# Optimization experiments

Measured on AMD Instinct MI355X. Metric: run time of the kernel, lower is better.

## Reference

```python
import jax, jax.numpy as jnp
import numpy as np

STRIDE = 1

def setup_inputs() -> dict:
    key = jax.random.key(0)
    k1, k2 = jax.random.split(key)
    x = jax.random.normal(k1, (16, 32, 32768), dtype=jnp.float32)
    # original uses torch.rand -> uniform [0,1)
    kernel = jax.random.uniform(k2, (1, 32, 32, 3), dtype=jnp.float32)
    return {"x": x, "kernel": kernel}

def reference(x, kernel):
    # Faithful intent of the module: strided valid 1D convolution.
    # x: (B, C_in, L); kernel: (1, C_out, C_in, K)
    w = kernel[0]  # (C_out, C_in, K)
    out = jax.lax.conv_general_dilated(
        x, w,
        window_strides=(STRIDE,),
        padding='VALID',
        dimension_numbers=('NCH', 'OIH', 'NCH'),
    )  # (B, C_out, (L-K)//STRIDE + 1)
    return out
```

## Files before the change

kernel.cpp:

```cpp
#include <hip/hip_runtime.h>

#define L_IN   32768
#define L_OUT  32766
#define C_IN   32
#define C_OUT  32
#define KW     3
#define TILE_L 128
#define TPB    4
#define NGRP   64
#define XROWS  130
#define PITCHW 32
#define LDSW   (XROWS * PITCHW)
#define WPLANE 3072

typedef __attribute__((ext_vector_type(8))) short bf16x8;
typedef __attribute__((ext_vector_type(4))) float f32x4;
typedef __attribute__((ext_vector_type(4))) unsigned int u32x4;

__device__ __forceinline__ unsigned pack_split(float v) {
    unsigned u = __float_as_uint(v);
    unsigned r = u + 0x7fffu + ((u >> 16) & 1u);
    float lo = v - __uint_as_float(r & 0xffff0000u);
    return (__float_as_uint(lo) & 0xffff0000u) | (r >> 16);
}

__device__ __forceinline__ unsigned prm(unsigned a, unsigned b, unsigned sel) {
    return __builtin_amdgcn_perm(a, b, sel);
}

__device__ __forceinline__ int lds_word(int l, int ci) {
    return l * PITCHW + ((((ci >> 2) ^ (l & 7)) << 2) | (ci & 3));
}

__global__ void prep_w(const float* __restrict__ w, unsigned short* __restrict__ wtf) {
    const int i = blockIdx.x * 256 + threadIdx.x;
    if (i >= 6 * 64 * 8) return;
    const int f    = i >> 9;
    const int rr   = i & 511;
    const int lane = rr >> 3;
    const int j    = rr & 7;
    const int kw   = f >> 1;
    const int cot  = f & 1;
    const int co   = cot * 16 + (lane & 15);
    const int ci   = (lane >> 4) * 8 + j;
    const float v  = w[(co * C_IN + ci) * KW + kw];
    unsigned u = __float_as_uint(v);
    unsigned r = u + 0x7fffu + ((u >> 16) & 1u);
    unsigned short hi = (unsigned short)(r >> 16);
    float lof = v - __uint_as_float(r & 0xffff0000u);
    unsigned lu = __float_as_uint(lof);
    unsigned lr = lu + 0x7fffu + ((lu >> 16) & 1u);
    unsigned short lo = (unsigned short)(lr >> 16);
    wtf[(f * 64 + lane) * 8 + j]          = hi;
    wtf[WPLANE + (f * 64 + lane) * 8 + j] = lo;
}

__global__ __launch_bounds__(256, 4) void conv1d_mfma(
    const float* __restrict__ x, const unsigned short* __restrict__ wtf,
    float* __restrict__ out)
{
    __shared__ __attribute__((aligned(16))) unsigned       xs[LDSW];
    __shared__ __attribute__((aligned(16))) unsigned short wl[2 * WPLANE];

    const int tid  = threadIdx.x;
    const int lane = tid & 63;
    const int wv   = tid >> 6;
    const int blk  = ((blockIdx.x & 7) << 7) | (blockIdx.x >> 3);
    const int bb   = blk >> 6;
    const int grp  = blk & (NGRP - 1);
    const int lg0  = grp * (TILE_L * TPB);

    const float* xb = x + (size_t)bb * C_IN * L_IN;

    {
        const u32x4* wsv = (const u32x4*)wtf;
        u32x4*       wdv = (u32x4*)wl;
#pragma unroll
        for (int i = 0; i < 3; ++i)
            wdv[tid * 3 + i] = wsv[tid * 3 + i];
    }

    const int c   = tid & 31;
    const int rr0 = tid >> 5;
    const int n   = lane & 15;
    const int kg  = lane >> 4;
    const int lb  = wv * 32;

    float sv[2][4][4];
    float hv[2];

    auto LOADT = [&](int l0, int s) {
#pragma unroll
        for (int r = 0; r < 4; ++r) {
            const float* src = xb + (size_t)(rr0 + r * 8) * L_IN + l0;
#pragma unroll
            for (int q = 0; q < 4; ++q)
                sv[s][r][q] = src[c + q * 32];
        }
        hv[s] = 0.f;
        if (tid < 64) {
            const int gl = l0 + TILE_L + (tid & 1);
            if (gl < L_IN) hv[s] = xb[(size_t)(tid >> 1) * L_IN + gl];
        }
        asm volatile("" ::: "memory");
    };
    auto WRITET = [&](int s) {
#pragma unroll
        for (int r = 0; r < 4; ++r)
#pragma unroll
            for (int q = 0; q < 4; ++q)
                xs[lds_word(c + q * 32, rr0 + r * 8)] = pack_split(sv[s][r][q]);
        if (tid < 64)
            xs[lds_word(TILE_L + (tid & 1), tid >> 1)] = pack_split(hv[s]);
    };

    LOADT(lg0, 0);
    LOADT(lg0 + TILE_L, 1);

    float* ob = out + (size_t)bb * C_OUT * L_OUT;

#pragma unroll
    for (int t = 0; t < TPB; ++t) {
        const int l0 = lg0 + t * TILE_L;
        WRITET(t & 1);
        if (t + 2 < TPB) LOADT(l0 + 2 * TILE_L, t & 1);
        __syncthreads();

        f32x4 acc[2][2];
#pragma unroll
        for (int a = 0; a < 2; ++a)
#pragma unroll
            for (int bq = 0; bq < 2; ++bq)
                acc[a][bq] = (f32x4){0.f, 0.f, 0.f, 0.f};

#pragma unroll
        for (int kw = 0; kw < KW; ++kw) {
            const int f0 = kw * 2, f1 = kw * 2 + 1;
            const bf16x8 ah0 = *(const bf16x8*)&wl[(f0 * 64 + lane) * 8];
            const bf16x8 al0 = *(const bf16x8*)&wl[WPLANE + (f0 * 64 + lane) * 8];
            const bf16x8 ah1 = *(const bf16x8*)&wl[(f1 * 64 + lane) * 8];
            const bf16x8 al1 = *(const bf16x8*)&wl[WPLANE + (f1 * 64 + lane) * 8];
#pragma unroll
            for (int lt = 0; lt < 2; ++lt) {
                const int lrow = lb + lt * 16 + n + kw;
                const int base = lrow * PITCHW;
                const int sw   = lrow & 7;
                const u32x4 pa = *(const u32x4*)&xs[base + (((kg * 2 + 0) ^ sw) << 2)];
                const u32x4 pb = *(const u32x4*)&xs[base + (((kg * 2 + 1) ^ sw) << 2)];
                u32x4 BH, BL;
                BH[0] = prm(pa[1], pa[0], 0x05040100u);
                BH[1] = prm(pa[3], pa[2], 0x05040100u);
                BH[2] = prm(pb[1], pb[0], 0x05040100u);
                BH[3] = prm(pb[3], pb[2], 0x05040100u);
                BL[0] = prm(pa[1], pa[0], 0x07060302u);
                BL[1] = prm(pa[3], pa[2], 0x07060302u);
                BL[2] = prm(pb[1], pb[0], 0x07060302u);
                BL[3] = prm(pb[3], pb[2], 0x07060302u);
                const bf16x8 bh = __builtin_bit_cast(bf16x8, BH);
                const bf16x8 bl = __builtin_bit_cast(bf16x8, BL);

                acc[0][lt] = __builtin_amdgcn_mfma_f32_16x16x32_bf16(ah0, bh, acc[0][lt], 0, 0, 0);
                acc[0][lt] = __builtin_amdgcn_mfma_f32_16x16x32_bf16(ah0, bl, acc[0][lt], 0, 0, 0);
                acc[0][lt] = __builtin_amdgcn_mfma_f32_16x16x32_bf16(al0, bh, acc[0][lt], 0, 0, 0);
                acc[1][lt] = __builtin_amdgcn_mfma_f32_16x16x32_bf16(ah1, bh, acc[1][lt], 0, 0, 0);
                acc[1][lt] = __builtin_amdgcn_mfma_f32_16x16x32_bf16(ah1, bl, acc[1][lt], 0, 0, 0);
                acc[1][lt] = __builtin_amdgcn_mfma_f32_16x16x32_bf16(al1, bh, acc[1][lt], 0, 0, 0);
            }
        }

        const int lw = l0 + lb;
        if (lw + 31 < L_OUT) {
#pragma unroll
            for (int cot = 0; cot < 2; ++cot)
#pragma unroll
                for (int lt = 0; lt < 2; ++lt) {
                    float* op = ob + (size_t)(cot * 16 + kg * 4) * L_OUT + lw + lt * 16 + n;
#pragma unroll
                    for (int r = 0; r < 4; ++r)
                        op[(size_t)r * L_OUT] = acc[cot][lt][r];
                }
        } else {
#pragma unroll
            for (int cot = 0; cot < 2; ++cot)
#pragma unroll
                for (int lt = 0; lt < 2; ++lt) {
                    const int l = lw + lt * 16 + n;
                    if (l < L_OUT) {
                        float* op = ob + (size_t)(cot * 16 + kg * 4) * L_OUT + l;
#pragma unroll
                        for (int r = 0; r < 4; ++r)
                            op[(size_t)r * L_OUT] = acc[cot][lt][r];
                    }
                }
        }

        if (t + 1 < TPB) __syncthreads();
    }
}

extern "C" void kernel_launch(void* const* d_in, const int* in_sizes, int n_in,
                              void* d_out, int out_size, void* d_ws, size_t ws_size,
                              hipStream_t stream) {
    const float* x = (const float*)d_in[0];
    const float* w = (const float*)d_in[1];
    float* out     = (float*)d_out;
    unsigned short* wtf = (unsigned short*)d_ws;

    prep_w<<<dim3(12), 256, 0, stream>>>(w, wtf);
    conv1d_mfma<<<dim3(16 * NGRP), 256, 0, stream>>>(x, wtf, out);
}
```

Baseline: 120.6 us.

## Drop weight low-bf16 plane, hoist weights to registers, halve tiles per block

Removes the third MFMA term (weight-lo times x-hi) so each output uses two bf16 products instead of three. Only the hi weight plane is staged in LDS, and the weights are loaded once into registers rather than once per tile. Tiles per block drop from 4 to 2 and the grid doubles, which also removes the in-loop prefetch of later tiles. Accuracy drops because the weights are now rounded to bf16, and the error may approach tolerance with 96-term sums of uniform weights.

Result: no change. 119.9 us (-0.6%).

```diff
diff --git a/kernel.cpp b/kernel.cpp
--- a/kernel.cpp
+++ b/kernel.cpp
@@ -6,8 +6,8 @@
 #define C_OUT  32
 #define KW     3
 #define TILE_L 128
-#define TPB    4
-#define NGRP   64
+#define TPB    2
+#define NGRP   128
 #define XROWS  130
 #define PITCHW 32
 #define LDSW   (XROWS * PITCHW)
@@ -60,24 +60,26 @@
     float* __restrict__ out)
 {
     __shared__ __attribute__((aligned(16))) unsigned       xs[LDSW];
-    __shared__ __attribute__((aligned(16))) unsigned short wl[2 * WPLANE];
+    __shared__ __attribute__((aligned(16))) unsigned short wl[WPLANE];
 
     const int tid  = threadIdx.x;
     const int lane = tid & 63;
     const int wv   = tid >> 6;
-    const int blk  = ((blockIdx.x & 7) << 7) | (blockIdx.x >> 3);
-    const int bb   = blk >> 6;
+    const int blk  = ((blockIdx.x & 7) << 8) | (blockIdx.x >> 3);
+    const int bb   = blk >> 7;
     const int grp  = blk & (NGRP - 1);
     const int lg0  = grp * (TILE_L * TPB);
 
     const float* xb = x + (size_t)bb * C_IN * L_IN;
 
     {
-        const u32x4* wsv = (const u32x4*)wtf;
-        u32x4*       wdv = (u32x4*)wl;
-#pragma unroll
-        for (int i = 0; i < 3; ++i)
-            wdv[tid * 3 + i] = wsv[tid * 3 + i];
+        const unsigned* wsv = (const unsigned*)wtf;
+        unsigned*       wdv = (unsigned*)wl;
+#pragma unroll
+        for (int i = 0; i < 6; ++i) {
+            const int idx = tid + i * 256;
+            wdv[idx] = wsv[idx];
+        }
     }
 
     const int c   = tid & 31;
@@ -116,14 +118,19 @@
 
     LOADT(lg0, 0);
     LOADT(lg0 + TILE_L, 1);
+    __syncthreads();
+
+    bf16x8 wa[6];
+#pragma unroll
+    for (int f = 0; f < 6; ++f)
+        wa[f] = *(const bf16x8*)&wl[(f * 64 + lane) * 8];
 
     float* ob = out + (size_t)bb * C_OUT * L_OUT;
 
 #pragma unroll
     for (int t = 0; t < TPB; ++t) {
         const int l0 = lg0 + t * TILE_L;
-        WRITET(t & 1);
-        if (t + 2 < TPB) LOADT(l0 + 2 * TILE_L, t & 1);
+        WRITET(t);
         __syncthreads();
 
         f32x4 acc[2][2];
@@ -136,10 +143,6 @@
 #pragma unroll
         for (int kw = 0; kw < KW; ++kw) {
             const int f0 = kw * 2, f1 = kw * 2 + 1;
-            const bf16x8 ah0 = *(const bf16x8*)&wl[(f0 * 64 + lane) * 8];
-            const bf16x8 al0 = *(const bf16x8*)&wl[WPLANE + (f0 * 64 + lane) * 8];
-            const bf16x8 ah1 = *(const bf16x8*)&wl[(f1 * 64 + lane) * 8];
-            const bf16x8 al1 = *(const bf16x8*)&wl[WPLANE + (f1 * 64 + lane) * 8];
 #pragma unroll
             for (int lt = 0; lt < 2; ++lt) {
                 const int lrow = lb + lt * 16 + n + kw;
@@ -159,12 +162,10 @@
                 const bf16x8 bh = __builtin_bit_cast(bf16x8, BH);
                 const bf16x8 bl = __builtin_bit_cast(bf16x8, BL);
 
-                acc[0][lt] = __builtin_amdgcn_mfma_f32_16x16x32_bf16(ah0, bh, acc[0][lt], 0, 0, 0);
-                acc[0][lt] = __builtin_amdgcn_mfma_f32_16x16x32_bf16(ah0, bl, acc[0][lt], 0, 0, 0);
-                acc[0][lt] = __builtin_amdgcn_mfma_f32_16x16x32_bf16(al0, bh, acc[0][lt], 0, 0, 0);
-                acc[1][lt] = __builtin_amdgcn_mfma_f32_16x16x32_bf16(ah1, bh, acc[1][lt], 0, 0, 0);
-                acc[1][lt] = __builtin_amdgcn_mfma_f32_16x16x32_bf16(ah1, bl, acc[1][lt], 0, 0, 0);
-                acc[1][lt] = __builtin_amdgcn_mfma_f32_16x16x32_bf16(al1, bh, acc[1][lt], 0, 0, 0);
+                acc[0][lt] = __builtin_amdgcn_mfma_f32_16x16x32_bf16(wa[f0], bh, acc[0][lt], 0, 0, 0);
+                acc[0][lt] = __builtin_amdgcn_mfma_f32_16x16x32_bf16(wa[f0], bl, acc[0][lt], 0, 0, 0);
+                acc[1][lt] = __builtin_amdgcn_mfma_f32_16x16x32_bf16(wa[f1], bh, acc[1][lt], 0, 0, 0);
+                acc[1][lt] = __builtin_amdgcn_mfma_f32_16x16x32_bf16(wa[f1], bl, acc[1][lt], 0, 0, 0);
             }
         }
 
```
